# Kernel optimization log

Hardware: AMD Instinct MI355X
Metric: run time of the kernel (lower is better)

The kernel has to match this reference:

```python
import jax, jax.numpy as jnp
import numpy as np

K, D, BETA = 512, 64, 0.25


def conv(x, w, b, s, p):
    # x: NCHW, w: OIHW (torch Conv2d layout)
    y = jax.lax.conv_general_dilated(x, w, (s, s), [(p, p), (p, p)],
                                     dimension_numbers=('NCHW', 'OIHW', 'NCHW'))
    if b is not None:
        y = y + b[None, :, None, None]
    return y


def conv_t(x, w, b, s, p):
    # torch ConvTranspose2d: w is (Cin, Cout, k, k). Equivalent to a dilated conv
    # with flipped, transposed kernel and padding k-1-p.
    k = w.shape[2]
    w2 = jnp.transpose(jnp.flip(w, (2, 3)), (1, 0, 2, 3))  # -> (Cout, Cin, k, k)
    y = jax.lax.conv_general_dilated(x, w2, (1, 1), [(k - 1 - p, k - 1 - p)] * 2,
                                     lhs_dilation=(s, s),
                                     dimension_numbers=('NCHW', 'OIHW', 'NCHW'))
    return y + b[None, :, None, None]


def res_stack(x, w1s, w2s):
    # w1s: (n_blocks, C_mid, C_in, 3, 3); w2s: (n_blocks, C_in, C_mid, 1, 1); no bias
    for i in range(w1s.shape[0]):
        h = conv(jax.nn.relu(x), w1s[i], None, 1, 1)
        h = conv(jax.nn.relu(h), w2s[i], None, 1, 0)
        x = x + h
    return jax.nn.relu(x)


def setup_inputs() -> dict:
    key = jax.random.key(0)
    ks = jax.random.split(key, 24)
    rn = lambda k, shape, s=0.05: (jax.random.normal(k, shape, jnp.float32) * s)
    return {
        'x': jax.random.normal(ks[0], (64, 3, 128, 128), jnp.float32),
        'enc_w1': rn(ks[1], (64, 3, 4, 4)),    'enc_b1': rn(ks[2], (64,)),
        'enc_w2': rn(ks[3], (128, 64, 4, 4)),  'enc_b2': rn(ks[4], (128,)),
        'enc_w3': rn(ks[5], (128, 128, 3, 3)), 'enc_b3': rn(ks[6], (128,)),
        'enc_w4': rn(ks[7], (128, 128, 3, 3)), 'enc_b4': rn(ks[8], (128,)),
        'enc_res_w1': rn(ks[9], (2, 64, 128, 3, 3)),
        'enc_res_w2': rn(ks[10], (2, 128, 64, 1, 1)),
        'enc_adj_w': rn(ks[11], (64, 128, 1, 1)), 'enc_adj_b': rn(ks[12], (64,)),
        'E': jax.random.uniform(ks[13], (K, D), jnp.float32, -1.0 / K, 1.0 / K),
        'dec_adj_w': rn(ks[14], (128, 64, 3, 3)), 'dec_adj_b': rn(ks[15], (128,)),
        'dec_res_w1': rn(ks[16], (2, 64, 128, 3, 3)),
        'dec_res_w2': rn(ks[17], (2, 128, 64, 1, 1)),
        'tc1_w': rn(ks[18], (128, 64, 4, 4)), 'tc1_b': rn(ks[19], (64,)),
        'tc2_w': rn(ks[20], (64, 3, 4, 4)),  'tc2_b': rn(ks[21], (3,)),
    }


def vq_vae_forward(x, enc_w1, enc_b1, enc_w2, enc_b2, enc_w3, enc_b3, enc_w4, enc_b4,
                   enc_res_w1, enc_res_w2, enc_adj_w, enc_adj_b, E,
                   dec_adj_w, dec_adj_b, dec_res_w1, dec_res_w2, tc1_w, tc1_b, tc2_w, tc2_b):
    relu = jax.nn.relu
    # ---- Encoder ----
    h = relu(conv(x, enc_w1, enc_b1, 2, 1))      # (B,64,64,64)
    h = relu(conv(h, enc_w2, enc_b2, 2, 1))      # (B,128,32,32)
    h = relu(conv(h, enc_w3, enc_b3, 1, 1))
    h = conv(h, enc_w4, enc_b4, 1, 1)
    h = res_stack(h, enc_res_w1, enc_res_w2)
    Ze = conv(h, enc_adj_w, enc_adj_b, 1, 0)     # (B,D,32,32)
    # ---- Vector quantizer (eval mode, use_EMA=False) ----
    Zt = jnp.transpose(Ze, (0, 2, 3, 1))          # (B,H,W,D)
    flat = Zt.reshape(-1, D)                      # (N,D), N=65536
    dist = (jnp.sum(flat ** 2, axis=1, keepdims=True)
            + jnp.sum(E ** 2, axis=1)
            - 2.0 * flat @ E.T)                    # (N,K)
    idx = jnp.argmin(dist, axis=1)                # (N,)
    Zq = E[idx].reshape(Zt.shape)
    e_latent_loss = jnp.mean((jax.lax.stop_gradient(Zq) - Zt) ** 2)
    q_latent_loss = jnp.mean((Zq - jax.lax.stop_gradient(Zt)) ** 2)
    e_and_q = q_latent_loss + BETA * e_latent_loss
    Zq_st = Zt + jax.lax.stop_gradient(Zq - Zt)   # straight-through
    Zq_nchw = jnp.transpose(Zq_st, (0, 3, 1, 2))
    counts = jnp.zeros((K,), jnp.float32).at[idx].add(1.0)
    probs = counts / jnp.sum(counts)
    entropy_bits = -jnp.sum(probs * jnp.log2(probs + 1e-10))  # zero-count terms vanish
    est_words = 2.0 ** entropy_bits
    # ---- Decoder ----
    g = conv(Zq_nchw, dec_adj_w, dec_adj_b, 1, 1)  # (B,128,32,32)
    g = res_stack(g, dec_res_w1, dec_res_w2)
    g = relu(conv_t(g, tc1_w, tc1_b, 2, 1))        # (B,64,64,64)
    x_recon = conv_t(g, tc2_w, tc2_b, 2, 1)        # (B,3,128,128)
    return e_and_q, x_recon, e_latent_loss, q_latent_loss, est_words


def reference(x, enc_w1, enc_b1, enc_w2, enc_b2, enc_w3, enc_b3, enc_w4, enc_b4,
              enc_res_w1, enc_res_w2, enc_adj_w, enc_adj_b, E,
              dec_adj_w, dec_adj_b, dec_res_w1, dec_res_w2, tc1_w, tc1_b, tc2_w, tc2_b):
    return vq_vae_forward(x, enc_w1, enc_b1, enc_w2, enc_b2, enc_w3, enc_b3, enc_w4, enc_b4,
                          enc_res_w1, enc_res_w2, enc_adj_w, enc_adj_b, E,
                          dec_adj_w, dec_adj_b, dec_res_w1, dec_res_w2, tc1_w, tc1_b, tc2_w, tc2_b)
```

## Files before the change

### kernel.cpp

```cpp
#include <hip/hip_runtime.h>
#include <math.h>


typedef unsigned short u16;
typedef __attribute__((ext_vector_type(8))) short bf16x8;
typedef __attribute__((ext_vector_type(4))) float f32x4;

__device__ __forceinline__ float bf2f(u16 h) {
    union { unsigned u; float f; } v; v.u = ((unsigned)h) << 16; return v.f;
}
__device__ __forceinline__ u16 f2bf(float f) {
    union { float f; unsigned u; } v; v.f = f;
    unsigned r = v.u + 0x7FFFu + ((v.u >> 16) & 1u);
    return (u16)(r >> 16);
}
__device__ __forceinline__ unsigned relu2(unsigned x) {
    return x & ~(((x & 0x80008000u) >> 15) * 0xFFFFu);
}

struct Taps { int s; int ntaps; int dh[16]; int dw[16]; };

template<int CIN, int COUT, bool RELU_IN, bool RELU_OUT, bool HAS_BIAS,
         bool RESID, bool PAR4>
__global__ __launch_bounds__(256)
void mfma_conv_k(const u16* __restrict__ in, const u16* __restrict__ wT,
                 const float* __restrict__ bias, u16* __restrict__ out,
                 int Hin, int Win, int Hout, int Wout, int OS, int OPH, int OPW,
                 Taps taps)
{
    constexpr int TM = 2, TN = 4;
    constexpr int LDA = 40;
    constexpr int NCH = CIN / 32;

    __shared__ alignas(16) u16 aT[128 * LDA];
    __shared__ alignas(16) u16 bT[64 * LDA];

    const int tid = threadIdx.x;
    const int m0 = blockIdx.x * 128;
    const int colbase = blockIdx.y << 6;
    const int pz = PAR4 ? blockIdx.z : 0;
    const int tapo = PAR4 ? pz * 4 : 0;
    const u16* wTb = PAR4 ? wT + (size_t)pz * 4 * COUT * CIN : wT;
    const int oph = PAR4 ? (pz >> 1) : OPH;
    const int opw = PAR4 ? (pz & 1) : OPW;
    const int n_img = m0 >> 10;
    const int pixbase = m0 & 1023;

    const int r = tid >> 1, half = tid & 1;
    const int pr = pixbase + r;
    const int ohr = pr >> 5, owr = pr & 31;
    const u16* inb = in + (size_t)n_img * Hin * Win * CIN;

    const int wv = tid >> 6, lane = tid & 63;
    const int q = lane >> 4, l16 = lane & 15;
    const int mbase = wv * 32;
    const bool bload = r < 64;

    f32x4 acc[TM][TN] = {};

    const int total_it = taps.ntaps * NCH;
    uint4 pa0, pa1, pb0 = {0,0,0,0}, pb1 = {0,0,0,0};

#define LOAD_IT(IT) do {                                                        \
        int t_ = (IT) / NCH, cc_ = ((IT) % NCH) * 32;                           \
        int ih_ = ohr * taps.s + taps.dh[tapo + t_];                            \
        int iw_ = owr * taps.s + taps.dw[tapo + t_];                            \
        bool ok_ = ((unsigned)ih_ < (unsigned)Hin) &&                           \
                   ((unsigned)iw_ < (unsigned)Win);                             \
        pa0 = (uint4){0,0,0,0}; pa1 = (uint4){0,0,0,0};                         \
        if (ok_) {                                                              \
            const u16* as_ = inb + ((size_t)ih_ * Win + iw_) * CIN              \
                             + half * 16 + cc_;                                 \
            pa0 = *(const uint4*)(as_);                                         \
            pa1 = *(const uint4*)(as_ + 8);                                     \
        }                                                                       \
        if (bload) {                                                            \
            const u16* bs_ = wTb + ((size_t)t_ * COUT + colbase + r) * CIN      \
                             + half * 16 + cc_;                                 \
            pb0 = *(const uint4*)(bs_);                                         \
            pb1 = *(const uint4*)(bs_ + 8);                                     \
        }                                                                       \
    } while (0)

    LOAD_IT(0);

    for (int it = 0; it < total_it; ++it) {
        __syncthreads();
        uint4 a0 = pa0, a1 = pa1;
        if (RELU_IN) {
            a0.x = relu2(a0.x); a0.y = relu2(a0.y); a0.z = relu2(a0.z); a0.w = relu2(a0.w);
            a1.x = relu2(a1.x); a1.y = relu2(a1.y); a1.z = relu2(a1.z); a1.w = relu2(a1.w);
        }
        *(uint4*)&aT[r * LDA + half * 16]     = a0;
        *(uint4*)&aT[r * LDA + half * 16 + 8] = a1;
        if (bload) {
            *(uint4*)&bT[r * LDA + half * 16]     = pb0;
            *(uint4*)&bT[r * LDA + half * 16 + 8] = pb1;
        }
        __syncthreads();
        if (it + 1 < total_it) LOAD_IT(it + 1);

        bf16x8 afr[TM], bfr[TN];
        #pragma unroll
        for (int tm = 0; tm < TM; ++tm)
            afr[tm] = *(const bf16x8*)&aT[(mbase + tm*16 + l16) * LDA + q * 8];
        #pragma unroll
        for (int tn = 0; tn < TN; ++tn)
            bfr[tn] = *(const bf16x8*)&bT[(tn*16 + l16) * LDA + q * 8];
        #pragma unroll
        for (int tm = 0; tm < TM; ++tm)
            #pragma unroll
            for (int tn = 0; tn < TN; ++tn)
                acc[tm][tn] = __builtin_amdgcn_mfma_f32_16x16x32_bf16(
                    afr[tm], bfr[tn], acc[tm][tn], 0, 0, 0);
    }
#undef LOAD_IT

    #pragma unroll
    for (int tm = 0; tm < TM; ++tm) {
        #pragma unroll
        for (int tn = 0; tn < TN; ++tn) {
            const int col = colbase + tn*16 + l16;
            const float bv = HAS_BIAS ? bias[col] : 0.0f;
            #pragma unroll
            for (int rg = 0; rg < 4; ++rg) {
                const int m = mbase + tm*16 + q*4 + rg;
                const int pix = pixbase + m;
                const int oh = pix >> 5, ow = pix & 31;
                size_t oidx = (((size_t)n_img * Hout + (oh*OS + oph)) * Wout
                               + (ow*OS + opw)) * COUT + col;
                float v = acc[tm][tn][rg] + bv;
                if (RESID) v += bf2f(out[oidx]);
                if (RELU_OUT) v = fmaxf(v, 0.0f);
                out[oidx] = f2bf(v);
            }
        }
    }
}

__global__ __launch_bounds__(256)
void res_fused_k(const u16* __restrict__ in, const u16* __restrict__ w1,
                 const u16* __restrict__ w2, u16* __restrict__ out)
{
    constexpr int LDA = 40;
    __shared__ alignas(16) u16 smem[20480];
    u16* aT   = smem;
    u16* bT   = smem + 5120;
    u16* mT0  = smem;
    u16* mT1  = smem + 5120;
    u16* b2T0 = smem + 10240;
    u16* b2T1 = smem + 15360;

    const int tid = threadIdx.x;
    const int m0 = blockIdx.x * 128;
    const int n_img = m0 >> 10;
    const int pixbase = m0 & 1023;

    const int r = tid >> 1, half = tid & 1;
    const int pr = pixbase + r;
    const int ohr = pr >> 5, owr = pr & 31;
    const u16* inb = in + (size_t)n_img * 1024 * 128;

    const int wv = tid >> 6, lane = tid & 63;
    const int q = lane >> 4, l16 = lane & 15;
    const int mbase = wv * 32;
    const bool bload = r < 64;

    {
        const u16* s = w2 + r * 64 + half * 32;
        u16* d = (half ? b2T1 : b2T0) + r * LDA;
        *(uint4*)(d)      = *(const uint4*)(s);
        *(uint4*)(d + 8)  = *(const uint4*)(s + 8);
        *(uint4*)(d + 16) = *(const uint4*)(s + 16);
        *(uint4*)(d + 24) = *(const uint4*)(s + 24);
    }

    f32x4 acc[2][4] = {};
    uint4 pa0, pa1, pb0 = {0,0,0,0}, pb1 = {0,0,0,0};

#define RLOAD(IT) do {                                                          \
        int t_ = (IT) >> 2, cc_ = ((IT) & 3) * 32;                              \
        int ih_ = ohr + t_/3 - 1, iw_ = owr + t_%3 - 1;                         \
        bool ok_ = ((unsigned)ih_ < 32u) && ((unsigned)iw_ < 32u);              \
        pa0 = (uint4){0,0,0,0}; pa1 = (uint4){0,0,0,0};                         \
        if (ok_) {                                                              \
            const u16* as_ = inb + ((size_t)ih_ * 32 + iw_) * 128               \
                             + half * 16 + cc_;                                 \
            pa0 = *(const uint4*)(as_);                                         \
            pa1 = *(const uint4*)(as_ + 8);                                     \
        }                                                                       \
        if (bload) {                                                            \
            const u16* bs_ = w1 + ((size_t)t_ * 64 + r) * 128                   \
                             + half * 16 + cc_;                                 \
            pb0 = *(const uint4*)(bs_);                                         \
            pb1 = *(const uint4*)(bs_ + 8);                                     \
        }                                                                       \
    } while (0)

    RLOAD(0);
    for (int it = 0; it < 36; ++it) {
        __syncthreads();
        uint4 a0 = pa0, a1 = pa1;
        a0.x = relu2(a0.x); a0.y = relu2(a0.y); a0.z = relu2(a0.z); a0.w = relu2(a0.w);
        a1.x = relu2(a1.x); a1.y = relu2(a1.y); a1.z = relu2(a1.z); a1.w = relu2(a1.w);
        *(uint4*)&aT[r * LDA + half * 16]     = a0;
        *(uint4*)&aT[r * LDA + half * 16 + 8] = a1;
        if (bload) {
            *(uint4*)&bT[r * LDA + half * 16]     = pb0;
            *(uint4*)&bT[r * LDA + half * 16 + 8] = pb1;
        }
        __syncthreads();
        if (it + 1 < 36) RLOAD(it + 1);

        bf16x8 afr[2], bfr[4];
        #pragma unroll
        for (int tm = 0; tm < 2; ++tm)
            afr[tm] = *(const bf16x8*)&aT[(mbase + tm*16 + l16) * LDA + q * 8];
        #pragma unroll
        for (int tn = 0; tn < 4; ++tn)
            bfr[tn] = *(const bf16x8*)&bT[(tn*16 + l16) * LDA + q * 8];
        #pragma unroll
        for (int tm = 0; tm < 2; ++tm)
            #pragma unroll
            for (int tn = 0; tn < 4; ++tn)
                acc[tm][tn] = __builtin_amdgcn_mfma_f32_16x16x32_bf16(
                    afr[tm], bfr[tn], acc[tm][tn], 0, 0, 0);
    }
#undef RLOAD

    __syncthreads();

    #pragma unroll
    for (int tm = 0; tm < 2; ++tm)
        #pragma unroll
        for (int tn = 0; tn < 4; ++tn) {
            u16* dst = (tn < 2) ? mT0 : mT1;
            const int kc = (tn & 1) * 16 + l16;
            #pragma unroll
            for (int rg = 0; rg < 4; ++rg) {
                int row = mbase + tm*16 + q*4 + rg;
                dst[row * LDA + kc] = f2bf(fmaxf(acc[tm][tn][rg], 0.0f));
            }
        }
    __syncthreads();

    f32x4 acc2[2][8] = {};
    #pragma unroll
    for (int kk = 0; kk < 2; ++kk) {
        const u16* mp = kk ? mT1 : mT0;
        const u16* bp = kk ? b2T1 : b2T0;
        bf16x8 af[2], bf[8];
        #pragma unroll
        for (int tm = 0; tm < 2; ++tm)
            af[tm] = *(const bf16x8*)&mp[(mbase + tm*16 + l16) * LDA + q * 8];
        #pragma unroll
        for (int tn = 0; tn < 8; ++tn)
            bf[tn] = *(const bf16x8*)&bp[(tn*16 + l16) * LDA + q * 8];
        #pragma unroll
        for (int tm = 0; tm < 2; ++tm)
            #pragma unroll
            for (int tn = 0; tn < 8; ++tn)
                acc2[tm][tn] = __builtin_amdgcn_mfma_f32_16x16x32_bf16(
                    af[tm], bf[tn], acc2[tm][tn], 0, 0, 0);
    }

    #pragma unroll
    for (int tm = 0; tm < 2; ++tm)
        #pragma unroll
        for (int tn = 0; tn < 8; ++tn) {
            const int col = tn*16 + l16;
            #pragma unroll
            for (int rg = 0; rg < 4; ++rg) {
                const int m = mbase + tm*16 + q*4 + rg;
                const int pix = pixbase + m;
                size_t off = ((size_t)n_img * 1024 + pix) * 128 + col;
                out[off] = f2bf(acc2[tm][tn][rg] + bf2f(in[off]));
            }
        }
}

__global__ __launch_bounds__(256)
void conv1_mfma_k(const float* __restrict__ x, const u16* __restrict__ wc1b,
                  const float* __restrict__ b, u16* __restrict__ out)
{
    __shared__ alignas(16) u16 smem[15360];
    u16* aT0 = smem;
    u16* aT1 = smem + 5120;
    u16* bT0 = smem + 10240;
    u16* bT1 = smem + 12800;

    const int tid = threadIdx.x;
    const int gbase = blockIdx.x * 128;
    const int r = tid >> 1, half = tid & 1;
    const int p = gbase + r;
    const int ow = p & 63, oh = (p >> 6) & 63, n = p >> 12;
    const float* xb = x + (size_t)n * 3 * 16384;

    {
        int row = tid >> 2, sub = tid & 3;
        *(uint4*)&bT0[row*40 + sub*8] = *(const uint4*)(wc1b + row*64 + sub*8);
        *(uint4*)&bT1[row*40 + sub*8] = *(const uint4*)(wc1b + row*64 + 32 + sub*8);
    }

    float vals[24];
    const int kb = half * 24;
    #pragma unroll
    for (int j = 0; j < 24; ++j) {
        int k = kb + j;
        int ci = k >> 4, kh = (k >> 2) & 3, kw = k & 3;
        int ih = oh*2 - 1 + kh, iw = ow*2 - 1 + kw;
        bool ok = ((unsigned)ih < 128u) && ((unsigned)iw < 128u);
        vals[j] = ok ? xb[ci*16384 + ih*128 + iw] : 0.0f;
    }
    unsigned pk[12];
    #pragma unroll
    for (int jj = 0; jj < 12; ++jj)
        pk[jj] = (unsigned)f2bf(vals[2*jj]) | ((unsigned)f2bf(vals[2*jj+1]) << 16);
    unsigned* a0row = (unsigned*)&aT0[r * 40];
    unsigned* a1row = (unsigned*)&aT1[r * 40];
    if (half == 0) {
        #pragma unroll
        for (int jj = 0; jj < 12; ++jj) a0row[jj] = pk[jj];
    } else {
        a0row[12] = pk[0]; a0row[13] = pk[1];
        a0row[14] = pk[2]; a0row[15] = pk[3];
        #pragma unroll
        for (int jj = 4; jj < 12; ++jj) a1row[jj - 4] = pk[jj];
        *(uint4*)&aT1[r*40 + 16] = (uint4){0,0,0,0};
        *(uint4*)&aT1[r*40 + 24] = (uint4){0,0,0,0};
    }
    __syncthreads();

    const int wv = tid >> 6, lane = tid & 63;
    const int q = lane >> 4, l16 = lane & 15;
    const int mbase = wv * 32;

    f32x4 acc[2][4] = {};
    bf16x8 af0[2], af1[2], bf0[4], bf1[4];
    #pragma unroll
    for (int tm = 0; tm < 2; ++tm) {
        af0[tm] = *(const bf16x8*)&aT0[(mbase + tm*16 + l16) * 40 + q * 8];
        af1[tm] = *(const bf16x8*)&aT1[(mbase + tm*16 + l16) * 40 + q * 8];
    }
    #pragma unroll
    for (int tn = 0; tn < 4; ++tn) {
        bf0[tn] = *(const bf16x8*)&bT0[(tn*16 + l16) * 40 + q * 8];
        bf1[tn] = *(const bf16x8*)&bT1[(tn*16 + l16) * 40 + q * 8];
    }
    #pragma unroll
    for (int tm = 0; tm < 2; ++tm)
        #pragma unroll
        for (int tn = 0; tn < 4; ++tn) {
            acc[tm][tn] = __builtin_amdgcn_mfma_f32_16x16x32_bf16(
                af0[tm], bf0[tn], acc[tm][tn], 0, 0, 0);
            acc[tm][tn] = __builtin_amdgcn_mfma_f32_16x16x32_bf16(
                af1[tm], bf1[tn], acc[tm][tn], 0, 0, 0);
        }

    float bv[4];
    #pragma unroll
    for (int tn = 0; tn < 4; ++tn) bv[tn] = b[tn*16 + l16];

    __syncthreads();
    u16* cbuf = smem;
    #pragma unroll
    for (int tm = 0; tm < 2; ++tm)
        #pragma unroll
        for (int tn = 0; tn < 4; ++tn)
            #pragma unroll
            for (int rg = 0; rg < 4; ++rg) {
                int row = mbase + tm*16 + q*4 + rg;
                int col = tn*16 + l16;
                cbuf[row*72 + col] = f2bf(fmaxf(acc[tm][tn][rg] + bv[tn], 0.0f));
            }
    __syncthreads();

    u16* ob = out + (size_t)gbase * 64;
    #pragma unroll
    for (int it = 0; it < 4; ++it) {
        int j = it * 256 + tid;
        uint4 v = *(const uint4*)&cbuf[(j >> 3) * 72 + (j & 7) * 8];
        *(uint4*)(ob + j * 8) = v;
    }
}

__global__ __launch_bounds__(256)
void tc2_mfma_k(const u16* __restrict__ in, const u16* __restrict__ wT,
                const float* __restrict__ bias, float* __restrict__ out)
{
    constexpr int LDA = 40;
    __shared__ alignas(16) u16 aT[128 * LDA];
    __shared__ alignas(16) u16 bT[16 * LDA];
    __shared__ float cT[128 * 17];

    const int tid = threadIdx.x;
    const int m0 = blockIdx.x * 128;
    const int n_img = m0 >> 12;
    const int pixbase = m0 & 4095;
    const int y0 = pixbase >> 6;

    const int r = tid >> 1, half = tid & 1;
    const int pr = pixbase + r;
    const int yr = pr >> 6, xr = pr & 63;
    const u16* inb = in + (size_t)n_img * 4096 * 64;

    const int wv = tid >> 6, lane = tid & 63;
    const int q = lane >> 4, l16 = lane & 15;
    const int mbase = wv * 32;

    f32x4 acc[2] = {};

    for (int t = 0; t < 9; ++t) {
        const int ih = yr + t/3 - 1;
        const int iw = xr + t%3 - 1;
        const bool ok = ((unsigned)ih < 64u) && ((unsigned)iw < 64u);
        const u16* asrc = ok ? (inb + ((size_t)ih * 64 + iw) * 64 + half * 16) : inb;
        const u16* bsrc = wT + ((size_t)t * 16 + r) * 64 + half * 16;

        for (int c0 = 0; c0 < 64; c0 += 32) {
            __syncthreads();
            uint4 a0 = {0,0,0,0}, a1 = {0,0,0,0};
            if (ok) {
                a0 = *(const uint4*)(asrc + c0);
                a1 = *(const uint4*)(asrc + c0 + 8);
            }
            *(uint4*)&aT[r * LDA + half * 16]     = a0;
            *(uint4*)&aT[r * LDA + half * 16 + 8] = a1;
            if (r < 16) {
                *(uint4*)&bT[r * LDA + half * 16]     = *(const uint4*)(bsrc + c0);
                *(uint4*)&bT[r * LDA + half * 16 + 8] = *(const uint4*)(bsrc + c0 + 8);
            }
            __syncthreads();

            bf16x8 af0 = *(const bf16x8*)&aT[(mbase + l16) * LDA + q * 8];
            bf16x8 af1 = *(const bf16x8*)&aT[(mbase + 16 + l16) * LDA + q * 8];
            bf16x8 bf  = *(const bf16x8*)&bT[l16 * LDA + q * 8];
            acc[0] = __builtin_amdgcn_mfma_f32_16x16x32_bf16(af0, bf, acc[0], 0, 0, 0);
            acc[1] = __builtin_amdgcn_mfma_f32_16x16x32_bf16(af1, bf, acc[1], 0, 0, 0);
        }
    }

    #pragma unroll
    for (int tm = 0; tm < 2; ++tm)
        #pragma unroll
        for (int rg = 0; rg < 4; ++rg)
            cT[(mbase + tm*16 + q*4 + rg) * 17 + l16] = acc[tm][rg];
    __syncthreads();

    #pragma unroll
    for (int it = 0; it < 6; ++it) {
        int j = it * 256 + tid;
        int co  = j >> 9;
        int rem = j & 511;
        int ohl = rem >> 7;
        int ow  = rem & 127;
        int oh  = 2*y0 + ohl;
        int lp  = (ohl >> 1) * 64 + (ow >> 1);
        int col = ((ohl & 1) * 2 + (ow & 1)) * 4 + co;
        float v = cT[lp * 17 + col] + bias[co];
        out[(((size_t)n_img * 3 + co) * 128 + oh) * 128 + ow] = v;
    }
}

__global__ __launch_bounds__(256)
void vq_mfma_k(const u16* __restrict__ Ze, const u16* __restrict__ Ebf,
               const float* __restrict__ enorm1, u16* __restrict__ Zq,
               u16* __restrict__ idx_out, float* __restrict__ sse)
{
    __shared__ alignas(16) u16 eld[256 * 72];
    __shared__ float en1s[256];
    __shared__ int bestk_s[128];
    __shared__ float red[256];

    const int tid = threadIdx.x;
    const int lane = tid & 63, wv = tid >> 6;
    const int q = lane >> 4, l16 = lane & 15;
    const int pb = blockIdx.x * 128 + wv * 32;

    bf16x8 alo[2], ahi[2];
    #pragma unroll
    for (int tile = 0; tile < 2; ++tile) {
        const u16* zp = Ze + (size_t)(pb + tile*16 + l16) * 64;
        alo[tile] = *(const bf16x8*)(zp + q * 8);
        ahi[tile] = *(const bf16x8*)(zp + 32 + q * 8);
    }

    unsigned key[2][4] = {{0xFFFFFFFFu,0xFFFFFFFFu,0xFFFFFFFFu,0xFFFFFFFFu},
                          {0xFFFFFFFFu,0xFFFFFFFFu,0xFFFFFFFFu,0xFFFFFFFFu}};

    for (int k0 = 0; k0 < 512; k0 += 256) {
        __syncthreads();
        const uint4* src = (const uint4*)(Ebf + k0 * 64);
        #pragma unroll
        for (int i = tid; i < 2048; i += 256) {
            int row = i >> 3, sub = i & 7;
            *(uint4*)&eld[row * 72 + sub * 8] = src[i];
        }
        en1s[tid] = enorm1[k0 + tid];
        __syncthreads();

        for (int t = 0; t < 16; ++t) {
            const int nl = t * 16 + l16;
            bf16x8 b0 = *(const bf16x8*)&eld[nl * 72 + q * 8];
            bf16x8 b1 = *(const bf16x8*)&eld[nl * 72 + 32 + q * 8];
            const float en1 = en1s[nl];
            const unsigned ng = (unsigned)(k0 + nl);
            #pragma unroll
            for (int tile = 0; tile < 2; ++tile) {
                f32x4 acc = {0.0f, 0.0f, 0.0f, 0.0f};
                acc = __builtin_amdgcn_mfma_f32_16x16x32_bf16(alo[tile], b0, acc, 0, 0, 0);
                acc = __builtin_amdgcn_mfma_f32_16x16x32_bf16(ahi[tile], b1, acc, 0, 0, 0);
                #pragma unroll
                for (int rg = 0; rg < 4; ++rg) {
                    float sc = fmaf(acc[rg], -2.0f, en1);
                    unsigned kk2 = (__float_as_uint(sc) & 0xFFFFFE00u) | ng;
                    key[tile][rg] = min(key[tile][rg], kk2);
                }
            }
        }
    }

    #pragma unroll
    for (int m = 1; m < 16; m <<= 1) {
        #pragma unroll
        for (int tile = 0; tile < 2; ++tile)
            #pragma unroll
            for (int rg = 0; rg < 4; ++rg) {
                unsigned o = (unsigned)__shfl_xor((int)key[tile][rg], m, 64);
                key[tile][rg] = min(key[tile][rg], o);
            }
    }
    if (l16 == 0) {
        #pragma unroll
        for (int tile = 0; tile < 2; ++tile)
            #pragma unroll
            for (int rg = 0; rg < 4; ++rg)
                bestk_s[wv * 32 + tile * 16 + q * 4 + rg] = (int)(key[tile][rg] & 511u);
    }
    __syncthreads();

    const int pos = tid >> 1, seg = tid & 1;
    const int p = blockIdx.x * 128 + pos;
    const int k = bestk_s[pos];
    const u16* ep = Ebf + (size_t)k * 64 + seg * 32;
    const u16* zp = Ze + (size_t)p * 64 + seg * 32;
    u16* qp = Zq + (size_t)p * 64 + seg * 32;
    float local = 0.0f;
    #pragma unroll
    for (int h = 0; h < 4; ++h) {
        uint4 ev = *(const uint4*)(ep + h * 8);
        uint4 zv = *(const uint4*)(zp + h * 8);
        *(uint4*)(qp + h * 8) = ev;
        unsigned ea[4] = {ev.x, ev.y, ev.z, ev.w};
        unsigned za[4] = {zv.x, zv.y, zv.z, zv.w};
        #pragma unroll
        for (int j = 0; j < 4; ++j) {
            float d0 = bf2f((u16)(ea[j] & 0xFFFFu)) - bf2f((u16)(za[j] & 0xFFFFu));
            float d1 = bf2f((u16)(ea[j] >> 16))     - bf2f((u16)(za[j] >> 16));
            local = fmaf(d0, d0, fmaf(d1, d1, local));
        }
    }
    if (seg == 0) idx_out[p] = (u16)k;
    red[tid] = local;
    __syncthreads();
    for (int s = 128; s > 0; s >>= 1) {
        if (tid < s) red[tid] += red[tid + s];
        __syncthreads();
    }
    if (tid == 0) atomicAdd(sse, red[0]);
}

__global__ __launch_bounds__(256)
void hist_k(const u16* __restrict__ idx, float* __restrict__ counts)
{
    __shared__ int red[256];
    const int k = blockIdx.x;
    const int tid = threadIdx.x;
    int c = 0;
    const uint4* p4 = (const uint4*)idx;
    for (int i = tid; i < 8192; i += 256) {
        uint4 v = p4[i];
        unsigned ua[4] = {v.x, v.y, v.z, v.w};
        #pragma unroll
        for (int j = 0; j < 4; ++j) {
            c += ((ua[j] & 0xFFFFu) == (unsigned)k);
            c += ((ua[j] >> 16)     == (unsigned)k);
        }
    }
    red[tid] = c;
    __syncthreads();
    for (int s = 128; s > 0; s >>= 1) {
        if (tid < s) red[tid] += red[tid + s];
        __syncthreads();
    }
    if (tid == 0) counts[k] = (float)red[0];
}

__device__ __forceinline__ void wconv_tf(const float* __restrict__ w,
                                         u16* __restrict__ o,
                                         int COUT, int CIN, int KK, int i)
{
    int ci = i % CIN; int t = i / CIN; int co = t % COUT; t /= COUT;
    o[i] = f2bf(w[(co*CIN + ci)*KK + t]);
}

__global__ __launch_bounds__(256)
void prep_k(const float* __restrict__ enc_w1, const float* __restrict__ enc_w2,
            const float* __restrict__ enc_w3, const float* __restrict__ enc_w4,
            const float* __restrict__ enc_res_w1, const float* __restrict__ enc_res_w2,
            const float* __restrict__ dec_res_w1, const float* __restrict__ dec_res_w2,
            const float* __restrict__ enc_adj_w, const float* __restrict__ dec_adj_w,
            const float* __restrict__ tc1_w, const float* __restrict__ tc2_w,
            const float* __restrict__ E,
            u16* __restrict__ wc1b, u16* __restrict__ wc2, u16* __restrict__ wc3,
            u16* __restrict__ wc4, u16* __restrict__ wer1, u16* __restrict__ wer2,
            u16* __restrict__ wdr1, u16* __restrict__ wdr2, u16* __restrict__ weadj,
            u16* __restrict__ wdadj, u16* __restrict__ wtc1, u16* __restrict__ wtc2b,
            u16* __restrict__ Ebf, float* __restrict__ enorm1, float* __restrict__ sse)
{
    const int b = blockIdx.x, tid = threadIdx.x;
    if (b < 512) {
        wconv_tf(enc_w2, wc2, 128, 64, 16, b * 256 + tid);
    } else if (b < 1088) {
        wconv_tf(enc_w3, wc3, 128, 128, 9, (b - 512) * 256 + tid);
    } else if (b < 1664) {
        wconv_tf(enc_w4, wc4, 128, 128, 9, (b - 1088) * 256 + tid);
    } else if (b < 2240) {
        int i = (b - 1664) * 256 + tid;
        int sub = i / 73728, rem = i - sub * 73728;
        wconv_tf(enc_res_w1 + sub * 73728, wer1 + sub * 73728, 64, 128, 9, rem);
    } else if (b < 2816) {
        int i = (b - 2240) * 256 + tid;
        int sub = i / 73728, rem = i - sub * 73728;
        wconv_tf(dec_res_w1 + sub * 73728, wdr1 + sub * 73728, 64, 128, 9, rem);
    } else if (b < 2880) {
        int i = (b - 2816) * 256 + tid;
        int sub = i >> 13, rem = i & 8191;
        wconv_tf(enc_res_w2 + sub * 8192, wer2 + sub * 8192, 128, 64, 1, rem);
    } else if (b < 2944) {
        int i = (b - 2880) * 256 + tid;
        int sub = i >> 13, rem = i & 8191;
        wconv_tf(dec_res_w2 + sub * 8192, wdr2 + sub * 8192, 128, 64, 1, rem);
    } else if (b < 2976) {
        wconv_tf(enc_adj_w, weadj, 64, 128, 1, (b - 2944) * 256 + tid);
    } else if (b < 3264) {
        wconv_tf(dec_adj_w, wdadj, 128, 64, 9, (b - 2976) * 256 + tid);
    } else if (b < 3776) {
        int i = (b - 3264) * 256 + tid;
        int ci = i & 127; int co = (i >> 7) & 63; int t = (i >> 13) & 3; int p = i >> 15;
        int poh = p >> 1, pw = p & 1; int a = t >> 1, bb = t & 1;
        int kh = poh ? (a ? 2 : 0) : (a ? 3 : 1);
        int kw = pw  ? (bb ? 2 : 0) : (bb ? 3 : 1);
        wtc1[i] = f2bf(tc1_w[((ci*64 + co)*4 + kh)*4 + kw]);
    } else if (b < 3812) {
        int i = (b - 3776) * 256 + tid;
        int ci = i & 63; int col = (i >> 6) & 15; int t = i >> 10;
        int dh = t / 3 - 1, dw = t % 3 - 1;
        int pp = col >> 2, co = col & 3;
        float v = 0.0f;
        if (co < 3) {
            int poh = pp >> 1, pw = pp & 1;
            int kh = poh ? (dh == 1 ? 0 : (dh == 0 ? 2 : -1))
                         : (dh == 0 ? 1 : (dh == -1 ? 3 : -1));
            int kw = pw  ? (dw == 1 ? 0 : (dw == 0 ? 2 : -1))
                         : (dw == 0 ? 1 : (dw == -1 ? 3 : -1));
            if (kh >= 0 && kw >= 0)
                v = tc2_w[((ci*3 + co)*4 + kh)*4 + kw];
        }
        wtc2b[i] = f2bf(v);
    } else if (b < 3814) {
        int k = (b - 3812) * 256 + tid;
        float s = 0.0f;
        #pragma unroll
        for (int d = 0; d < 64; ++d) {
            u16 h = f2bf(E[k*64 + d]);
            Ebf[k*64 + d] = h;
            float v = bf2f(h);
            s = fmaf(v, v, s);
        }
        enorm1[k] = s + 1.0f;
    } else if (b < 3830) {
        int i = (b - 3814) * 256 + tid;
        int co = i >> 6, k = i & 63;
        float v = 0.0f;
        if (k < 48) {
            int ci = k >> 4, kh = (k >> 2) & 3, kw = k & 3;
            v = enc_w1[((co*3 + ci)*4 + kh)*4 + kw];
        }
        wc1b[i] = f2bf(v);
    } else {
        if (tid == 0) sse[0] = 0.0f;
    }
}

__global__ void finalize_k(const float* __restrict__ counts, const float* __restrict__ sse,
                           float* __restrict__ out_head, float* __restrict__ out_tail)
{
    __shared__ float red[512];
    int t = threadIdx.x;
    float pr = counts[t] / 65536.0f;
    red[t] = -pr * log2f(pr + 1e-10f);
    __syncthreads();
    for (int s = 256; s > 0; s >>= 1) {
        if (t < s) red[t] += red[t + s];
        __syncthreads();
    }
    if (t == 0) {
        float entropy = red[0];
        float mse = sse[0] / 4194304.0f;
        out_head[0] = 1.25f * mse;
        out_tail[0] = mse;
        out_tail[1] = mse;
        out_tail[2] = exp2f(entropy);
    }
}

extern "C" void kernel_launch(void* const* d_in, const int* in_sizes, int n_in,
                              void* d_out, int out_size, void* d_ws, size_t ws_size,
                              hipStream_t stream)
{
    const float* x         = (const float*)d_in[0];
    const float* enc_w1    = (const float*)d_in[1];
    const float* enc_b1    = (const float*)d_in[2];
    const float* enc_w2    = (const float*)d_in[3];
    const float* enc_b2    = (const float*)d_in[4];
    const float* enc_w3    = (const float*)d_in[5];
    const float* enc_b3    = (const float*)d_in[6];
    const float* enc_w4    = (const float*)d_in[7];
    const float* enc_b4    = (const float*)d_in[8];
    const float* enc_res_w1= (const float*)d_in[9];
    const float* enc_res_w2= (const float*)d_in[10];
    const float* enc_adj_w = (const float*)d_in[11];
    const float* enc_adj_b = (const float*)d_in[12];
    const float* Ecb       = (const float*)d_in[13];
    const float* dec_adj_w = (const float*)d_in[14];
    const float* dec_adj_b = (const float*)d_in[15];
    const float* dec_res_w1= (const float*)d_in[16];
    const float* dec_res_w2= (const float*)d_in[17];
    const float* tc1_w     = (const float*)d_in[18];
    const float* tc1_b     = (const float*)d_in[19];
    const float* tc2_w     = (const float*)d_in[20];
    const float* tc2_b     = (const float*)d_in[21];

    char* wsb = (char*)d_ws;
    u16*   wc2   = (u16*)(wsb + 0);
    u16*   wc3   = (u16*)(wsb + 262144);
    u16*   wc4   = (u16*)(wsb + 557056);
    u16*   wer1  = (u16*)(wsb + 851968);
    u16*   wer2  = (u16*)(wsb + 1146880);
    u16*   weadj = (u16*)(wsb + 1179648);
    u16*   wdadj = (u16*)(wsb + 1196032);
    u16*   wdr1  = (u16*)(wsb + 1343488);
    u16*   wdr2  = (u16*)(wsb + 1638400);
    u16*   wtc1  = (u16*)(wsb + 1671168);
    u16*   wtc2b = (u16*)(wsb + 1933312);
    float* counts= (float*)(wsb + 1951744);
    float* sse   = counts + 512;
    u16*   Ebf   = (u16*)(wsb + 1955840);
    float* enorm1= (float*)(wsb + 2021376);
    u16*   wc1b  = (u16*)(wsb + 2023424);
    u16*   H1    = (u16*)(wsb + 2097152);
    u16*   TR    = (u16*)(wsb + 35651584);
    u16*   H3    = (u16*)(wsb + 52428800);
    u16*   ZE    = (u16*)(wsb + 77594624);
    u16*   ZQ    = (u16*)(wsb + 85983232);
    u16*   IDX   = (u16*)(wsb + 94371840);
    u16*   TC1O  = H1;

    float* out  = (float*)d_out;
    float* xrec = out + 1;
    float* tail = out + 1 + 3145728;

    Taps t3x3; t3x3.s = 1; t3x3.ntaps = 9;
    for (int kh = 0; kh < 3; ++kh) for (int kw = 0; kw < 3; ++kw) {
        t3x3.dh[kh*3+kw] = kh - 1; t3x3.dw[kh*3+kw] = kw - 1;
    }
    Taps t1x1; t1x1.s = 1; t1x1.ntaps = 1; t1x1.dh[0] = 0; t1x1.dw[0] = 0;
    Taps t4x4; t4x4.s = 2; t4x4.ntaps = 16;
    for (int kh = 0; kh < 4; ++kh) for (int kw = 0; kw < 4; ++kw) {
        t4x4.dh[kh*4+kw] = kh - 1; t4x4.dw[kh*4+kw] = kw - 1;
    }
    const int dtab[2][2] = {{0, -1}, {1, 0}};
    Taps ttc1m; ttc1m.s = 1; ttc1m.ntaps = 4;
    for (int p = 0; p < 4; ++p)
        for (int a = 0; a < 2; ++a) for (int bb = 0; bb < 2; ++bb) {
            ttc1m.dh[p*4 + a*2 + bb] = dtab[p>>1][a];
            ttc1m.dw[p*4 + a*2 + bb] = dtab[p&1][bb];
        }

    prep_k<<<3831, 256, 0, stream>>>(enc_w1, enc_w2, enc_w3, enc_w4,
        enc_res_w1, enc_res_w2, dec_res_w1, dec_res_w2, enc_adj_w, dec_adj_w,
        tc1_w, tc2_w, Ecb, wc1b, wc2, wc3, wc4, wer1, wer2, wdr1, wdr2,
        weadj, wdadj, wtc1, wtc2b, Ebf, enorm1, sse);

    conv1_mfma_k<<<2048, 256, 0, stream>>>(x, wc1b, enc_b1, H1);
    mfma_conv_k<64,128,false,true,true,false,false><<<dim3(512,2), 256, 0, stream>>>
        (H1, wc2, enc_b2, TR, 64, 64, 32, 32, 1, 0, 0, t4x4);
    mfma_conv_k<128,128,false,true,true,false,false><<<dim3(512,2), 256, 0, stream>>>
        (TR, wc3, enc_b3, H3, 32, 32, 32, 32, 1, 0, 0, t3x3);
    mfma_conv_k<128,128,false,false,true,false,false><<<dim3(512,2), 256, 0, stream>>>
        (H3, wc4, enc_b4, TR, 32, 32, 32, 32, 1, 0, 0, t3x3);
    res_fused_k<<<512, 256, 0, stream>>>(TR, wer1,         wer2,        H3);
    res_fused_k<<<512, 256, 0, stream>>>(H3, wer1 + 73728, wer2 + 8192, TR);
    mfma_conv_k<128,64,true,false,true,false,false><<<dim3(512,1), 256, 0, stream>>>
        (TR, weadj, enc_adj_b, ZE, 32, 32, 32, 32, 1, 0, 0, t1x1);

    vq_mfma_k<<<512, 256, 0, stream>>>(ZE, Ebf, enorm1, ZQ, IDX, sse);
    hist_k<<<512, 256, 0, stream>>>(IDX, counts);

    mfma_conv_k<64,128,false,false,true,false,false><<<dim3(512,2), 256, 0, stream>>>
        (ZQ, wdadj, dec_adj_b, H3, 32, 32, 32, 32, 1, 0, 0, t3x3);
    res_fused_k<<<512, 256, 0, stream>>>(H3, wdr1,         wdr2,        TR);
    res_fused_k<<<512, 256, 0, stream>>>(TR, wdr1 + 73728, wdr2 + 8192, H3);
    mfma_conv_k<128,64,true,true,true,false,true><<<dim3(512,1,4), 256, 0, stream>>>
        (H3, wtc1, tc1_b, TC1O, 32, 32, 64, 64, 2, 0, 0, ttc1m);
    tc2_mfma_k<<<2048, 256, 0, stream>>>(TC1O, wtc2b, tc2_b, xrec);

    finalize_k<<<1, 512, 0, stream>>>(counts, sse, out, tail);
}
```

Baseline: 463.5 us.

## Fuse encoder 1x1 adjust conv into VQ kernel and compile-time conv taps

Merges the 1x1 encoder adjust convolution with the vector-quantization search into one kernel. The latent stays in shared memory and is never written to or read back from global memory. The SSE is computed algebraically as |z|^2 + min score - 1 instead of re-reading Ze, which relies on the codebook norm term being folded into enorm1 and may shift rounding. The conv kernel also replaces runtime tap tables passed as kernel arguments with compile-time tap modes, which removes per-iteration table lookups.

```diff
diff --git a/kernel.cpp b/kernel.cpp
--- a/kernel.cpp
+++ b/kernel.cpp
@@ -18,19 +18,19 @@
     return x & ~(((x & 0x80008000u) >> 15) * 0xFFFFu);
 }
 
-struct Taps { int s; int ntaps; int dh[16]; int dw[16]; };
-
-template<int CIN, int COUT, bool RELU_IN, bool RELU_OUT, bool HAS_BIAS,
-         bool RESID, bool PAR4>
+template<int CIN, int COUT, int TAPMODE, bool RELU_IN, bool RELU_OUT,
+         bool HAS_BIAS, bool RESID>
 __global__ __launch_bounds__(256)
 void mfma_conv_k(const u16* __restrict__ in, const u16* __restrict__ wT,
                  const float* __restrict__ bias, u16* __restrict__ out,
-                 int Hin, int Win, int Hout, int Wout, int OS, int OPH, int OPW,
-                 Taps taps)
+                 int Hin, int Win, int Hout, int Wout, int OS)
 {
     constexpr int TM = 2, TN = 4;
     constexpr int LDA = 40;
     constexpr int NCH = CIN / 32;
+    constexpr int NTAPS = (TAPMODE == 0) ? 1 : (TAPMODE == 1) ? 9
+                        : (TAPMODE == 2) ? 16 : 4;
+    constexpr int S = (TAPMODE == 2) ? 2 : 1;
 
     __shared__ alignas(16) u16 aT[128 * LDA];
     __shared__ alignas(16) u16 bT[64 * LDA];
@@ -38,11 +38,10 @@
     const int tid = threadIdx.x;
     const int m0 = blockIdx.x * 128;
     const int colbase = blockIdx.y << 6;
-    const int pz = PAR4 ? blockIdx.z : 0;
-    const int tapo = PAR4 ? pz * 4 : 0;
-    const u16* wTb = PAR4 ? wT + (size_t)pz * 4 * COUT * CIN : wT;
-    const int oph = PAR4 ? (pz >> 1) : OPH;
-    const int opw = PAR4 ? (pz & 1) : OPW;
+    const int pz = (TAPMODE == 3) ? blockIdx.z : 0;
+    const u16* wTb = (TAPMODE == 3) ? wT + (size_t)pz * 4 * COUT * CIN : wT;
+    const int oph = (TAPMODE == 3) ? (pz >> 1) : 0;
+    const int opw = (TAPMODE == 3) ? (pz & 1) : 0;
     const int n_img = m0 >> 10;
     const int pixbase = m0 & 1023;
 
@@ -58,13 +57,18 @@
 
     f32x4 acc[TM][TN] = {};
 
-    const int total_it = taps.ntaps * NCH;
+    const int total_it = NTAPS * NCH;
     uint4 pa0, pa1, pb0 = {0,0,0,0}, pb1 = {0,0,0,0};
 
 #define LOAD_IT(IT) do {                                                        \
         int t_ = (IT) / NCH, cc_ = ((IT) % NCH) * 32;                           \
-        int ih_ = ohr * taps.s + taps.dh[tapo + t_];                            \
-        int iw_ = owr * taps.s + taps.dw[tapo + t_];                            \
+        int dh_, dw_;                                                           \
+        if (TAPMODE == 0)      { dh_ = 0;              dw_ = 0; }               \
+        else if (TAPMODE == 1) { dh_ = t_/3 - 1;       dw_ = t_%3 - 1; }        \
+        else if (TAPMODE == 2) { dh_ = (t_>>2) - 1;    dw_ = (t_&3) - 1; }      \
+        else                   { dh_ = (pz>>1) - (t_>>1); dw_ = (pz&1) - (t_&1); } \
+        int ih_ = ohr * S + dh_;                                                \
+        int iw_ = owr * S + dw_;                                                \
         bool ok_ = ((unsigned)ih_ < (unsigned)Hin) &&                           \
                    ((unsigned)iw_ < (unsigned)Win);                             \
         pa0 = (uint4){0,0,0,0}; pa1 = (uint4){0,0,0,0};                         \
@@ -280,6 +284,190 @@
 }
 
 __global__ __launch_bounds__(256)
+void adjvq_k(const u16* __restrict__ TRin, const u16* __restrict__ wadj,
+             const float* __restrict__ bias, const u16* __restrict__ Ebf,
+             const float* __restrict__ enorm1, u16* __restrict__ Zq,
+             u16* __restrict__ idx_out, float* __restrict__ sse)
+{
+    constexpr int LDA = 40;
+    __shared__ alignas(16) u16 smem[18432];
+    u16* aT  = smem;
+    u16* bT  = smem + 5120;
+    u16* mT0 = smem;
+    u16* mT1 = smem + 5120;
+    u16* eld = smem;
+    __shared__ float znorm_s[128];
+    __shared__ float bestf_s[128];
+    __shared__ float en1s[256];
+    __shared__ int   bestk_s[128];
+    __shared__ float red[256];
+
+    const int tid = threadIdx.x;
+    const int r = tid >> 1, half = tid & 1;
+    const size_t gp = (size_t)blockIdx.x * 128 + r;
+    const u16* arow = TRin + gp * 128 + half * 16;
+    const u16* brow = wadj + (size_t)r * 128 + half * 16;
+
+    const int wv = tid >> 6, lane = tid & 63;
+    const int q = lane >> 4, l16 = lane & 15;
+    const int mbase = wv * 32;
+
+    f32x4 acc[2][4] = {};
+    for (int c0 = 0; c0 < 128; c0 += 32) {
+        __syncthreads();
+        uint4 a0 = *(const uint4*)(arow + c0);
+        uint4 a1 = *(const uint4*)(arow + c0 + 8);
+        a0.x = relu2(a0.x); a0.y = relu2(a0.y); a0.z = relu2(a0.z); a0.w = relu2(a0.w);
+        a1.x = relu2(a1.x); a1.y = relu2(a1.y); a1.z = relu2(a1.z); a1.w = relu2(a1.w);
+        *(uint4*)&aT[r * LDA + half * 16]     = a0;
+        *(uint4*)&aT[r * LDA + half * 16 + 8] = a1;
+        if (r < 64) {
+            *(uint4*)&bT[r * LDA + half * 16]     = *(const uint4*)(brow + c0);
+            *(uint4*)&bT[r * LDA + half * 16 + 8] = *(const uint4*)(brow + c0 + 8);
+        }
+        __syncthreads();
+        bf16x8 afr[2], bfr[4];
+        #pragma unroll
+        for (int tm = 0; tm < 2; ++tm)
+            afr[tm] = *(const bf16x8*)&aT[(mbase + tm*16 + l16) * LDA + q * 8];
+        #pragma unroll
+        for (int tn = 0; tn < 4; ++tn)
+            bfr[tn] = *(const bf16x8*)&bT[(tn*16 + l16) * LDA + q * 8];
+        #pragma unroll
+        for (int tm = 0; tm < 2; ++tm)
+            #pragma unroll
+            for (int tn = 0; tn < 4; ++tn)
+                acc[tm][tn] = __builtin_amdgcn_mfma_f32_16x16x32_bf16(
+                    afr[tm], bfr[tn], acc[tm][tn], 0, 0, 0);
+    }
+
+    float zn[2][4] = {};
+    #pragma unroll
+    for (int tm = 0; tm < 2; ++tm)
+        #pragma unroll
+        for (int tn = 0; tn < 4; ++tn) {
+            const float bv = bias[tn*16 + l16];
+            #pragma unroll
+            for (int rg = 0; rg < 4; ++rg) {
+                float z = acc[tm][tn][rg] + bv;
+                acc[tm][tn][rg] = z;
+                zn[tm][rg] = fmaf(z, z, zn[tm][rg]);
+            }
+        }
+    #pragma unroll
+    for (int m = 1; m < 16; m <<= 1)
+        #pragma unroll
+        for (int tm = 0; tm < 2; ++tm)
+            #pragma unroll
+            for (int rg = 0; rg < 4; ++rg)
+                zn[tm][rg] += __shfl_xor(zn[tm][rg], m, 64);
+
+    __syncthreads();
+
+    #pragma unroll
+    for (int tm = 0; tm < 2; ++tm) {
+        #pragma unroll
+        for (int tn = 0; tn < 4; ++tn) {
+            u16* dst = (tn < 2) ? mT0 : mT1;
+            const int kc = (tn & 1) * 16 + l16;
+            #pragma unroll
+            for (int rg = 0; rg < 4; ++rg) {
+                int row = mbase + tm*16 + q*4 + rg;
+                dst[row * LDA + kc] = f2bf(acc[tm][tn][rg]);
+            }
+        }
+        if (l16 == 0)
+            #pragma unroll
+            for (int rg = 0; rg < 4; ++rg)
+                znorm_s[mbase + tm*16 + q*4 + rg] = zn[tm][rg];
+    }
+    __syncthreads();
+
+    bf16x8 alo[2], ahi[2];
+    #pragma unroll
+    for (int tile = 0; tile < 2; ++tile) {
+        alo[tile] = *(const bf16x8*)&mT0[(mbase + tile*16 + l16) * LDA + q * 8];
+        ahi[tile] = *(const bf16x8*)&mT1[(mbase + tile*16 + l16) * LDA + q * 8];
+    }
+
+    unsigned key[2][4] = {{0xFFFFFFFFu,0xFFFFFFFFu,0xFFFFFFFFu,0xFFFFFFFFu},
+                          {0xFFFFFFFFu,0xFFFFFFFFu,0xFFFFFFFFu,0xFFFFFFFFu}};
+    float fb[2][4] = {{1e30f,1e30f,1e30f,1e30f},{1e30f,1e30f,1e30f,1e30f}};
+
+    for (int k0 = 0; k0 < 512; k0 += 256) {
+        __syncthreads();
+        const uint4* src = (const uint4*)(Ebf + k0 * 64);
+        #pragma unroll
+        for (int i = tid; i < 2048; i += 256) {
+            int row = i >> 3, sub = i & 7;
+            *(uint4*)&eld[row * 72 + sub * 8] = src[i];
+        }
+        en1s[tid] = enorm1[k0 + tid];
+        __syncthreads();
+
+        for (int t = 0; t < 16; ++t) {
+            const int nl = t * 16 + l16;
+            bf16x8 b0 = *(const bf16x8*)&eld[nl * 72 + q * 8];
+            bf16x8 b1 = *(const bf16x8*)&eld[nl * 72 + 32 + q * 8];
+            const float en1 = en1s[nl];
+            const unsigned ng = (unsigned)(k0 + nl);
+            #pragma unroll
+            for (int tile = 0; tile < 2; ++tile) {
+                f32x4 sc4 = {0.0f, 0.0f, 0.0f, 0.0f};
+                sc4 = __builtin_amdgcn_mfma_f32_16x16x32_bf16(alo[tile], b0, sc4, 0, 0, 0);
+                sc4 = __builtin_amdgcn_mfma_f32_16x16x32_bf16(ahi[tile], b1, sc4, 0, 0, 0);
+                #pragma unroll
+                for (int rg = 0; rg < 4; ++rg) {
+                    float sc = fmaf(sc4[rg], -2.0f, en1);
+                    unsigned kk2 = (__float_as_uint(sc) & 0xFFFFFE00u) | ng;
+                    key[tile][rg] = min(key[tile][rg], kk2);
+                    fb[tile][rg] = fminf(fb[tile][rg], sc);
+                }
+            }
+        }
+    }
+
+    #pragma unroll
+    for (int m = 1; m < 16; m <<= 1)
+        #pragma unroll
+        for (int tile = 0; tile < 2; ++tile)
+            #pragma unroll
+            for (int rg = 0; rg < 4; ++rg) {
+                unsigned o = (unsigned)__shfl_xor((int)key[tile][rg], m, 64);
+                key[tile][rg] = min(key[tile][rg], o);
+                float of = __shfl_xor(fb[tile][rg], m, 64);
+                fb[tile][rg] = fminf(fb[tile][rg], of);
+            }
+    if (l16 == 0)
+        #pragma unroll
+        for (int tile = 0; tile < 2; ++tile)
+            #pragma unroll
+            for (int rg = 0; rg < 4; ++rg) {
+                int row = mbase + tile*16 + q*4 + rg;
+                bestk_s[row] = (int)(key[tile][rg] & 511u);
+                bestf_s[row] = fb[tile][rg];
+            }
+    __syncthreads();
+
+    const int pos = tid >> 1, seg = tid & 1;
+    const size_t p = (size_t)blockIdx.x * 128 + pos;
+    const int k = bestk_s[pos];
+    const u16* ep = Ebf + (size_t)k * 64 + seg * 32;
+    u16* qp = Zq + p * 64 + seg * 32;
+    #pragma unroll
+    for (int h = 0; h < 4; ++h)
+        *(uint4*)(qp + h * 8) = *(const uint4*)(ep + h * 8);
+    if (seg == 0) idx_out[p] = (u16)k;
+    red[tid] = (seg == 0) ? (znorm_s[pos] + bestf_s[pos] - 1.0f) : 0.0f;
+    __syncthreads();
+    for (int s = 128; s > 0; s >>= 1) {
+        if (tid < s) red[tid] += red[tid + s];
+        __syncthreads();
+    }
+    if (tid == 0) atomicAdd(sse, red[0]);
+}
+
+__global__ __launch_bounds__(256)
 void conv1_mfma_k(const float* __restrict__ x, const u16* __restrict__ wc1b,
                   const float* __restrict__ b, u16* __restrict__ out)
 {
@@ -460,114 +648,6 @@
         float v = cT[lp * 17 + col] + bias[co];
         out[(((size_t)n_img * 3 + co) * 128 + oh) * 128 + ow] = v;
     }
-}
-
-__global__ __launch_bounds__(256)
-void vq_mfma_k(const u16* __restrict__ Ze, const u16* __restrict__ Ebf,
-               const float* __restrict__ enorm1, u16* __restrict__ Zq,
-               u16* __restrict__ idx_out, float* __restrict__ sse)
-{
-    __shared__ alignas(16) u16 eld[256 * 72];
-    __shared__ float en1s[256];
-    __shared__ int bestk_s[128];
-    __shared__ float red[256];
-
-    const int tid = threadIdx.x;
-    const int lane = tid & 63, wv = tid >> 6;
-    const int q = lane >> 4, l16 = lane & 15;
-    const int pb = blockIdx.x * 128 + wv * 32;
-
-    bf16x8 alo[2], ahi[2];
-    #pragma unroll
-    for (int tile = 0; tile < 2; ++tile) {
-        const u16* zp = Ze + (size_t)(pb + tile*16 + l16) * 64;
-        alo[tile] = *(const bf16x8*)(zp + q * 8);
-        ahi[tile] = *(const bf16x8*)(zp + 32 + q * 8);
-    }
-
-    unsigned key[2][4] = {{0xFFFFFFFFu,0xFFFFFFFFu,0xFFFFFFFFu,0xFFFFFFFFu},
-                          {0xFFFFFFFFu,0xFFFFFFFFu,0xFFFFFFFFu,0xFFFFFFFFu}};
-
-    for (int k0 = 0; k0 < 512; k0 += 256) {
-        __syncthreads();
-        const uint4* src = (const uint4*)(Ebf + k0 * 64);
-        #pragma unroll
-        for (int i = tid; i < 2048; i += 256) {
-            int row = i >> 3, sub = i & 7;
-            *(uint4*)&eld[row * 72 + sub * 8] = src[i];
-        }
-        en1s[tid] = enorm1[k0 + tid];
-        __syncthreads();
-
-        for (int t = 0; t < 16; ++t) {
-            const int nl = t * 16 + l16;
-            bf16x8 b0 = *(const bf16x8*)&eld[nl * 72 + q * 8];
-            bf16x8 b1 = *(const bf16x8*)&eld[nl * 72 + 32 + q * 8];
-            const float en1 = en1s[nl];
-            const unsigned ng = (unsigned)(k0 + nl);
-            #pragma unroll
-            for (int tile = 0; tile < 2; ++tile) {
-                f32x4 acc = {0.0f, 0.0f, 0.0f, 0.0f};
-                acc = __builtin_amdgcn_mfma_f32_16x16x32_bf16(alo[tile], b0, acc, 0, 0, 0);
-                acc = __builtin_amdgcn_mfma_f32_16x16x32_bf16(ahi[tile], b1, acc, 0, 0, 0);
-                #pragma unroll
-                for (int rg = 0; rg < 4; ++rg) {
-                    float sc = fmaf(acc[rg], -2.0f, en1);
-                    unsigned kk2 = (__float_as_uint(sc) & 0xFFFFFE00u) | ng;
-                    key[tile][rg] = min(key[tile][rg], kk2);
-                }
-            }
-        }
-    }
-
-    #pragma unroll
-    for (int m = 1; m < 16; m <<= 1) {
-        #pragma unroll
-        for (int tile = 0; tile < 2; ++tile)
-            #pragma unroll
-            for (int rg = 0; rg < 4; ++rg) {
-                unsigned o = (unsigned)__shfl_xor((int)key[tile][rg], m, 64);
-                key[tile][rg] = min(key[tile][rg], o);
-            }
-    }
-    if (l16 == 0) {
-        #pragma unroll
-        for (int tile = 0; tile < 2; ++tile)
-            #pragma unroll
-            for (int rg = 0; rg < 4; ++rg)
-                bestk_s[wv * 32 + tile * 16 + q * 4 + rg] = (int)(key[tile][rg] & 511u);
-    }
-    __syncthreads();
-
-    const int pos = tid >> 1, seg = tid & 1;
-    const int p = blockIdx.x * 128 + pos;
-    const int k = bestk_s[pos];
-    const u16* ep = Ebf + (size_t)k * 64 + seg * 32;
-    const u16* zp = Ze + (size_t)p * 64 + seg * 32;
-    u16* qp = Zq + (size_t)p * 64 + seg * 32;
-    float local = 0.0f;
-    #pragma unroll
-    for (int h = 0; h < 4; ++h) {
-        uint4 ev = *(const uint4*)(ep + h * 8);
-        uint4 zv = *(const uint4*)(zp + h * 8);
-        *(uint4*)(qp + h * 8) = ev;
-        unsigned ea[4] = {ev.x, ev.y, ev.z, ev.w};
-        unsigned za[4] = {zv.x, zv.y, zv.z, zv.w};
-        #pragma unroll
-        for (int j = 0; j < 4; ++j) {
-            float d0 = bf2f((u16)(ea[j] & 0xFFFFu)) - bf2f((u16)(za[j] & 0xFFFFu));
-            float d1 = bf2f((u16)(ea[j] >> 16))     - bf2f((u16)(za[j] >> 16));
-            local = fmaf(d0, d0, fmaf(d1, d1, local));
-        }
-    }
-    if (seg == 0) idx_out[p] = (u16)k;
-    red[tid] = local;
-    __syncthreads();
-    for (int s = 128; s > 0; s >>= 1) {
-        if (tid < s) red[tid] += red[tid + s];
-        __syncthreads();
-    }
-    if (tid == 0) atomicAdd(sse, red[0]);
 }
 
 __global__ __launch_bounds__(256)
@@ -762,7 +842,6 @@
     u16*   H1    = (u16*)(wsb + 2097152);
     u16*   TR    = (u16*)(wsb + 35651584);
     u16*   H3    = (u16*)(wsb + 52428800);
-    u16*   ZE    = (u16*)(wsb + 77594624);
     u16*   ZQ    = (u16*)(wsb + 85983232);
     u16*   IDX   = (u16*)(wsb + 94371840);
     u16*   TC1O  = H1;
@@ -770,23 +849,6 @@
     float* out  = (float*)d_out;
     float* xrec = out + 1;
     float* tail = out + 1 + 3145728;
-
-    Taps t3x3; t3x3.s = 1; t3x3.ntaps = 9;
-    for (int kh = 0; kh < 3; ++kh) for (int kw = 0; kw < 3; ++kw) {
-        t3x3.dh[kh*3+kw] = kh - 1; t3x3.dw[kh*3+kw] = kw - 1;
-    }
-    Taps t1x1; t1x1.s = 1; t1x1.ntaps = 1; t1x1.dh[0] = 0; t1x1.dw[0] = 0;
-    Taps t4x4; t4x4.s = 2; t4x4.ntaps = 16;
-    for (int kh = 0; kh < 4; ++kh) for (int kw = 0; kw < 4; ++kw) {
-        t4x4.dh[kh*4+kw] = kh - 1; t4x4.dw[kh*4+kw] = kw - 1;
-    }
-    const int dtab[2][2] = {{0, -1}, {1, 0}};
-    Taps ttc1m; ttc1m.s = 1; ttc1m.ntaps = 4;
-    for (int p = 0; p < 4; ++p)
-        for (int a = 0; a < 2; ++a) for (int bb = 0; bb < 2; ++bb) {
-            ttc1m.dh[p*4 + a*2 + bb] = dtab[p>>1][a];
-            ttc1m.dw[p*4 + a*2 + bb] = dtab[p&1][bb];
-        }
 
     prep_k<<<3831, 256, 0, stream>>>(enc_w1, enc_w2, enc_w3, enc_w4,
         enc_res_w1, enc_res_w2, dec_res_w1, dec_res_w2, enc_adj_w, dec_adj_w,
@@ -794,26 +856,25 @@
         weadj, wdadj, wtc1, wtc2b, Ebf, enorm1, sse);
 
     conv1_mfma_k<<<2048, 256, 0, stream>>>(x, wc1b, enc_b1, H1);
-    mfma_conv_k<64,128,false,true,true,false,false><<<dim3(512,2), 256, 0, stream>>>
-        (H1, wc2, enc_b2, TR, 64, 64, 32, 32, 1, 0, 0, t4x4);
-    mfma_conv_k<128,128,false,true,true,false,false><<<dim3(512,2), 256, 0, stream>>>
-        (TR, wc3, enc_b3, H3, 32, 32, 32, 32, 1, 0, 0, t3x3);
-    mfma_conv_k<128,128,false,false,true,false,false><<<dim3(512,2), 256, 0, stream>>>
-        (H3, wc4, enc_b4, TR, 32, 32, 32, 32, 1, 0, 0, t3x3);
+    mfma_conv_k<64,128,2,false,true,true,false><<<dim3(512,2), 256, 0, stream>>>
+        (H1, wc2, enc_b2, TR, 64, 64, 32, 32, 1);
+    mfma_conv_k<128,128,1,false,true,true,false><<<dim3(512,2), 256, 0, stream>>>
+        (TR, wc3, enc_b3, H3, 32, 32, 32, 32, 1);
+    mfma_conv_k<128,128,1,false,false,true,false><<<dim3(512,2), 256, 0, stream>>>
+        (H3, wc4, enc_b4, TR, 32, 32, 32, 32, 1);
     res_fused_k<<<512, 256, 0, stream>>>(TR, wer1,         wer2,        H3);
     res_fused_k<<<512, 256, 0, stream>>>(H3, wer1 + 73728, wer2 + 8192, TR);
-    mfma_conv_k<128,64,true,false,true,false,false><<<dim3(512,1), 256, 0, stream>>>
-        (TR, weadj, enc_adj_b, ZE, 32, 32, 32, 32, 1, 0, 0, t1x1);
-
-    vq_mfma_k<<<512, 256, 0, stream>>>(ZE, Ebf, enorm1, ZQ, IDX, sse);
+
+    adjvq_k<<<512, 256, 0, stream>>>(TR, weadj, enc_adj_b, Ebf, enorm1,
+                                     ZQ, IDX, sse);
     hist_k<<<512, 256, 0, stream>>>(IDX, counts);
 
-    mfma_conv_k<64,128,false,false,true,false,false><<<dim3(512,2), 256, 0, stream>>>
-        (ZQ, wdadj, dec_adj_b, H3, 32, 32, 32, 32, 1, 0, 0, t3x3);
+    mfma_conv_k<64,128,1,false,false,true,false><<<dim3(512,2), 256, 0, stream>>>
+        (ZQ, wdadj, dec_adj_b, H3, 32, 32, 32, 32, 1);
     res_fused_k<<<512, 256, 0, stream>>>(H3, wdr1,         wdr2,        TR);
     res_fused_k<<<512, 256, 0, stream>>>(TR, wdr1 + 73728, wdr2 + 8192, H3);
-    mfma_conv_k<128,64,true,true,true,false,true><<<dim3(512,1,4), 256, 0, stream>>>
-        (H3, wtc1, tc1_b, TC1O, 32, 32, 64, 64, 2, 0, 0, ttc1m);
+    mfma_conv_k<128,64,3,true,true,true,false><<<dim3(512,1,4), 256, 0, stream>>>
+        (H3, wtc1, tc1_b, TC1O, 32, 32, 64, 64, 2);
     tc2_mfma_k<<<2048, 256, 0, stream>>>(TC1O, wtc2b, tc2_b, xrec);
 
     finalize_k<<<1, 512, 0, stream>>>(counts, sse, out, tail);
```

After: 453.9 us. 1.02x faster.
